# Performance work log

Hardware: AMD Instinct MI355X
Metric: run time of the kernel (lower is better)

The kernel has to match this reference:

```python
import jax, jax.numpy as jnp
import numpy as np

B, T, D = 16, 4096, 768          # batch, tokens, hidden
N_BOX = 1024                      # total boxes across batch
MAX_BBOX = 128                    # cfg.MODEL.MAX_BBOX_NUM
DIM_DETR = 256                    # DETR feature dim (features[:,1:])


def _lin(k, din, dout):
    kw, kb = jax.random.split(k)
    s = 1.0 / np.sqrt(din)
    W = jax.random.uniform(kw, (dout, din), minval=-s, maxval=s, dtype=jnp.float32)
    b = jax.random.uniform(kb, (dout,), minval=-s, maxval=s, dtype=jnp.float32)
    return W, b


def setup_inputs() -> dict:
    key = jax.random.key(0)
    ks = jax.random.split(key, 10)
    inputs = jax.random.normal(ks[0], (B, T, D), dtype=jnp.float32)
    img = jnp.sort(jax.random.randint(ks[1], (N_BOX,), 0, B))
    rest = jax.random.randint(ks[2], (N_BOX, 4), 0, 224)
    bboxes = jnp.concatenate([img[:, None], rest], axis=1).astype(jnp.int32)
    features = jax.random.normal(ks[3], (N_BOX, 1 + DIM_DETR), dtype=jnp.float32)
    t1w, t1b = _lin(ks[4], D, D)      # transform layer 1
    t2w, t2b = _lin(ks[5], D, D)      # transform layer 2
    d1w, d1b = _lin(ks[6], D, D)      # deep_trans layer 1
    d2w, d2b = _lin(ks[7], D, D)      # deep_trans layer 2
    k8a, k8b = jax.random.split(ks[8])
    m1w, m1b = _lin(k8a, DIM_DETR, D) # mlp layer 1 (256->768)
    m2w, m2b = _lin(k8b, D, D)        # mlp layer 2
    pw, pb = _lin(ks[9], 2 * D, D)    # projection (1536->768)
    return dict(inputs=inputs, bboxes=bboxes, features=features,
                t1w=t1w, t1b=t1b, t2w=t2w, t2b=t2b,
                d1w=d1w, d1b=d1b, d2w=d2w, d2b=d2b,
                m1w=m1w, m1b=m1b, m2w=m2w, m2b=m2b,
                pw=pw, pb=pb)


def reference(inputs, bboxes, features, t1w, t1b, t2w, t2b,
              d1w, d1b, d2w, d2b, m1w, m1b, m2w, m2b, pw, pb):
    x = inputs.mean(axis=1)                                    # [B, D]
    ret_x = jax.nn.relu(x @ d1w.T + d1b) @ d2w.T + d2b         # deep_trans
    xt = jax.nn.relu(x @ t1w.T + t1b) @ t2w.T + t2b            # transform
    img = bboxes[:, 0]                                          # [N] image idx per box
    x_boxes = xt[img]                                           # broadcast image feat to its boxes
    fm = jax.nn.relu(features[:, 1:] @ m1w.T + m1b) @ m2w.T + m2b  # DETR mlp
    h = jnp.concatenate([x_boxes, fm], axis=1) @ pw.T + pb      # [N, D]
    # ragged pad: scatter each box into slot (img, rank-within-image)
    counts = jax.ops.segment_sum(jnp.ones((N_BOX,), jnp.int32), img, num_segments=B)
    offsets = jnp.cumsum(counts) - counts                       # exclusive cumsum (boxes sorted by img)
    pos = jnp.arange(N_BOX) - offsets[img]
    vis_output = jnp.zeros((B, MAX_BBOX, D), h.dtype).at[img, pos].set(h)
    att_mask = (jnp.arange(MAX_BBOX)[None, :] < counts[:, None]).astype(jnp.float32)
    return vis_output, att_mask, ret_x
```

## Files before the change

kernel.cpp:

```cpp
#include <hip/hip_runtime.h>

#define B_ 16
#define T_ 4096
#define D_ 768
#define NBOX 1024
#define MAXBB 128
#define DDETR 256

typedef unsigned short u16;
typedef short bf16x8 __attribute__((ext_vector_type(8)));
typedef float f32x4 __attribute__((ext_vector_type(4)));

__device__ __forceinline__ void split_bf(float f, u16& h, u16& l) {
    unsigned u = __builtin_bit_cast(unsigned, f);
    unsigned r = u + 0x7fffu + ((u >> 16) & 1u);
    u16 hb = (u16)(r >> 16);
    float hf = __builtin_bit_cast(float, (unsigned)hb << 16);
    float lf = f - hf;
    unsigned ul = __builtin_bit_cast(unsigned, lf);
    unsigned rl = ul + 0x7fffu + ((ul >> 16) & 1u);
    h = hb; l = (u16)(rl >> 16);
}

__global__ __launch_bounds__(192) void k_mean_partial(const float4* __restrict__ in4,
                                                      float4* __restrict__ part4) {
    int blk = blockIdx.x;
    int b = blk >> 6, c = blk & 63;
    int t = threadIdx.x;
    const float4* base = in4 + (size_t)b * (T_ * D_ / 4) + (size_t)c * (64 * D_ / 4);
    float4 s = {0.f, 0.f, 0.f, 0.f};
    #pragma unroll 4
    for (int r = 0; r < 64; ++r) {
        float4 v = base[(size_t)r * 192 + t];
        s.x += v.x; s.y += v.y; s.z += v.z; s.w += v.w;
    }
    part4[(size_t)blk * 192 + t] = s;
}

__global__ __launch_bounds__(96) void k_mean_final_pack(const float* __restrict__ part,
                                                        u16* __restrict__ xph, u16* __restrict__ xpl) {
    int b = blockIdx.x;
    int kc = threadIdx.x;
    f32x4 s0 = {0,0,0,0}, s1 = {0,0,0,0};
    for (int c = 0; c < 64; ++c) {
        const float* p = part + ((size_t)(b * 64 + c)) * D_ + kc * 8;
        s0 += *(const f32x4*)p;
        s1 += *(const f32x4*)(p + 4);
    }
    const float inv = 1.0f / T_;
    bf16x8 hv, lv;
    #pragma unroll
    for (int j = 0; j < 4; ++j) {
        u16 h, l;
        split_bf(s0[j] * inv, h, l); hv[j] = (short)h; lv[j] = (short)l;
        split_bf(s1[j] * inv, h, l); hv[4 + j] = (short)h; lv[4 + j] = (short)l;
    }
    size_t off = ((size_t)kc * 16 + b) * 8;
    *(bf16x8*)(xph + off) = hv;
    *(bf16x8*)(xpl + off) = lv;
}

struct WDesc { const float* src; u16* hi; u16* lo; int N; int K; };
struct WPack7 { WDesc d[7]; };

__global__ __launch_bounds__(256) void k_pack_w(WPack7 ws) {
    WDesc d = ws.d[blockIdx.y];
    int idx = blockIdx.x * 256 + threadIdx.x;
    int Kc = d.K >> 3;
    int total = d.N * Kc;
    if (idx >= total) return;
    int n = idx / Kc, kc = idx - n * Kc;
    const float* s = d.src + (size_t)n * d.K + kc * 8;
    f32x4 v0 = *(const f32x4*)s, v1 = *(const f32x4*)(s + 4);
    bf16x8 hv, lv;
    #pragma unroll
    for (int j = 0; j < 4; ++j) {
        u16 h, l;
        split_bf(v0[j], h, l); hv[j] = (short)h; lv[j] = (short)l;
        split_bf(v1[j], h, l); hv[4 + j] = (short)h; lv[4 + j] = (short)l;
    }
    size_t off = ((size_t)(n >> 4) * Kc + kc) * 128 + (n & 15) * 8;
    *(bf16x8*)(d.hi + off) = hv;
    *(bf16x8*)(d.lo + off) = lv;
}

__global__ __launch_bounds__(256) void k_pack_feat(const float* __restrict__ feat,
                                                   u16* __restrict__ fh, u16* __restrict__ fl) {
    int idx = blockIdx.x * 256 + threadIdx.x;
    if (idx >= NBOX * 32) return;
    int i = idx >> 5, kc = idx & 31;
    const float* s = feat + (size_t)i * 257 + 1 + kc * 8;
    bf16x8 hv, lv;
    #pragma unroll
    for (int j = 0; j < 8; ++j) {
        u16 h, l;
        split_bf(s[j], h, l); hv[j] = (short)h; lv[j] = (short)l;
    }
    size_t off = ((size_t)(i >> 4) * 32 + kc) * 128 + (i & 15) * 8;
    *(bf16x8*)(fh + off) = hv;
    *(bf16x8*)(fl + off) = lv;
}

__global__ __launch_bounds__(256) void k_mfma(const u16* __restrict__ Ahi, const u16* __restrict__ Alo,
                                              const u16* __restrict__ Whi, const u16* __restrict__ Wlo,
                                              float* __restrict__ P, int Kc, int kcLen, int nks) {
    int z = blockIdx.z;
    int term = z / nks, ks = z - term * nks;
    const u16* A = (term == 2) ? Alo : Ahi;
    const u16* W = (term == 1) ? Wlo : Whi;
    int lane = threadIdx.x & 63, w = threadIdx.x >> 6;
    int wm = w >> 1, wn = w & 1;
    int mt0 = blockIdx.y * 8 + wm * 4;
    int nt0 = blockIdx.x * 8 + wn * 4;
    int kc0 = ks * kcLen;
    int nk = kcLen >> 2;

    const u16* Ap = A + ((size_t)mt0 * Kc + kc0) * 128 + lane * 8;
    const u16* Wp = W + ((size_t)nt0 * Kc + kc0) * 128 + lane * 8;
    size_t astr = (size_t)Kc * 128;

    bf16x8 a[4], b[4];
    #pragma unroll
    for (int i = 0; i < 4; ++i) {
        a[i] = *(const bf16x8*)(Ap + i * astr);
        b[i] = *(const bf16x8*)(Wp + i * astr);
    }
    f32x4 acc[16];
    #pragma unroll
    for (int i = 0; i < 16; ++i) acc[i] = (f32x4){0.f, 0.f, 0.f, 0.f};

    for (int k = 0; k < nk; ++k) {
        bf16x8 an[4], bn[4];
        if (k + 1 < nk) {
            #pragma unroll
            for (int i = 0; i < 4; ++i) {
                an[i] = *(const bf16x8*)(Ap + i * astr + (size_t)(k + 1) * 512);
                bn[i] = *(const bf16x8*)(Wp + i * astr + (size_t)(k + 1) * 512);
            }
        }
        #pragma unroll
        for (int i = 0; i < 4; ++i)
            #pragma unroll
            for (int j = 0; j < 4; ++j)
                acc[i * 4 + j] = __builtin_amdgcn_mfma_f32_16x16x32_bf16(a[i], b[j], acc[i * 4 + j], 0, 0, 0);
        #pragma unroll
        for (int i = 0; i < 4; ++i) { a[i] = an[i]; b[i] = bn[i]; }
    }

    float* Pz = P + (size_t)z * (1024 * 768);
    int rb = (lane >> 4) * 4, cb = lane & 15;
    #pragma unroll
    for (int i = 0; i < 4; ++i)
        #pragma unroll
        for (int j = 0; j < 4; ++j) {
            int row = (mt0 + i) * 16 + rb;
            int col = (nt0 + j) * 16 + cb;
            float* p = Pz + (size_t)row * 768 + col;
            f32x4 v = acc[i * 4 + j];
            #pragma unroll
            for (int r = 0; r < 4; ++r) p[(size_t)r * 768] = v[r];
        }
}

template<int RELU>
__global__ __launch_bounds__(256) void k_epi_pack(const float* __restrict__ P, int NS,
                                                  const float* __restrict__ bias,
                                                  u16* __restrict__ dhi, u16* __restrict__ dlo,
                                                  int KcDst, int kcOff) {
    int idx = blockIdx.x * 256 + threadIdx.x;
    int m = idx / 96, kc = idx - m * 96;
    const float* p0 = P + (size_t)m * 768 + kc * 8;
    f32x4 s0 = *(const f32x4*)p0, s1 = *(const f32x4*)(p0 + 4);
    for (int z = 1; z < NS; ++z) {
        const float* p = p0 + (size_t)z * (1024 * 768);
        s0 += *(const f32x4*)p; s1 += *(const f32x4*)(p + 4);
    }
    s0 += *(const f32x4*)(bias + kc * 8);
    s1 += *(const f32x4*)(bias + kc * 8 + 4);
    bf16x8 hv, lv;
    #pragma unroll
    for (int j = 0; j < 4; ++j) {
        float v0 = RELU ? fmaxf(s0[j], 0.f) : s0[j];
        float v1 = RELU ? fmaxf(s1[j], 0.f) : s1[j];
        u16 h, l;
        split_bf(v0, h, l); hv[j] = (short)h; lv[j] = (short)l;
        split_bf(v1, h, l); hv[4 + j] = (short)h; lv[4 + j] = (short)l;
    }
    size_t off = ((size_t)(m >> 4) * KcDst + kcOff + kc) * 128 + (m & 15) * 8;
    *(bf16x8*)(dhi + off) = hv;
    *(bf16x8*)(dlo + off) = lv;
}

__global__ __launch_bounds__(256) void k_epi_f32(const float* __restrict__ P, int NS,
                                                 const float* __restrict__ bias,
                                                 float* __restrict__ C) {
    int idx = blockIdx.x * 256 + threadIdx.x;
    int m = idx / 192, c4 = idx - m * 192;
    size_t off = (size_t)m * 768 + c4 * 4;
    f32x4 s = *(const f32x4*)(P + off);
    for (int z = 1; z < NS; ++z) s += *(const f32x4*)(P + (size_t)z * (1024 * 768) + off);
    s += *(const f32x4*)(bias + c4 * 4);
    *(f32x4*)(C + off) = s;
}

__global__ __launch_bounds__(256) void k_small(const u16* __restrict__ A0h, const u16* __restrict__ A0l,
                                               const u16* __restrict__ A1h, const u16* __restrict__ A1l,
                                               const u16* __restrict__ W0h, const u16* __restrict__ W0l,
                                               const u16* __restrict__ W1h, const u16* __restrict__ W1l,
                                               float* __restrict__ Ps) {
    int z = blockIdx.y;
    int term = z >> 2, ks = z & 3;
    int lane = threadIdx.x & 63, w = threadIdx.x >> 6;
    int nt0 = blockIdx.x * 16 + w * 4;
    int path = nt0 >= 48;
    int ntp = nt0 - path * 48;
    const u16* Ah = path ? A1h : A0h;
    const u16* Al = path ? A1l : A0l;
    const u16* Wh = path ? W1h : W0h;
    const u16* Wl = path ? W1l : W0l;
    const u16* A = (term == 2) ? Al : Ah;
    const u16* W = (term == 1) ? Wl : Wh;
    int kc0 = ks * 24;

    const u16* Ap = A + (size_t)kc0 * 128 + lane * 8;
    const u16* Wp = W + ((size_t)ntp * 96 + kc0) * 128 + lane * 8;

    f32x4 acc[4];
    #pragma unroll
    for (int i = 0; i < 4; ++i) acc[i] = (f32x4){0.f, 0.f, 0.f, 0.f};

    #pragma unroll
    for (int k = 0; k < 6; ++k) {
        bf16x8 a = *(const bf16x8*)(Ap + (size_t)k * 512);
        bf16x8 b[4];
        #pragma unroll
        for (int j = 0; j < 4; ++j)
            b[j] = *(const bf16x8*)(Wp + (size_t)j * 96 * 128 + (size_t)k * 512);
        #pragma unroll
        for (int j = 0; j < 4; ++j)
            acc[j] = __builtin_amdgcn_mfma_f32_16x16x32_bf16(a, b[j], acc[j], 0, 0, 0);
    }

    float* Pz = Ps + (size_t)z * (16 * 1536);
    int rb = (lane >> 4) * 4, cb = lane & 15;
    #pragma unroll
    for (int j = 0; j < 4; ++j) {
        int col = (nt0 + j) * 16 + cb;
        float* p = Pz + (size_t)rb * 1536 + col;
        f32x4 v = acc[j];
        #pragma unroll
        for (int r = 0; r < 4; ++r) p[(size_t)r * 1536] = v[r];
    }
}

__global__ __launch_bounds__(256) void k_sepi1(const float* __restrict__ Ps,
                                               const float* __restrict__ d1b, const float* __restrict__ t1b,
                                               u16* __restrict__ xh, u16* __restrict__ xl) {
    int idx = blockIdx.x * 256 + threadIdx.x;
    int r = idx / 192, cc = idx - r * 192;
    size_t base = (size_t)r * 1536 + cc * 8;
    f32x4 s0 = {0,0,0,0}, s1 = {0,0,0,0};
    for (int z = 0; z < 12; ++z) {
        const float* p = Ps + (size_t)z * (16 * 1536) + base;
        s0 += *(const f32x4*)p; s1 += *(const f32x4*)(p + 4);
    }
    int path = cc >= 96;
    int ccp = cc - path * 96;
    const float* bias = (path ? t1b : d1b) + ccp * 8;
    s0 += *(const f32x4*)bias;
    s1 += *(const f32x4*)(bias + 4);
    bf16x8 hv, lv;
    #pragma unroll
    for (int j = 0; j < 4; ++j) {
        u16 h, l;
        split_bf(fmaxf(s0[j], 0.f), h, l); hv[j] = (short)h; lv[j] = (short)l;
        split_bf(fmaxf(s1[j], 0.f), h, l); hv[4 + j] = (short)h; lv[4 + j] = (short)l;
    }
    size_t off = (size_t)path * 12288 + (size_t)ccp * 128 + r * 8;
    *(bf16x8*)(xh + off) = hv;
    *(bf16x8*)(xl + off) = lv;
}

__global__ __launch_bounds__(256) void k_sepi2(const float* __restrict__ Ps,
                                               const float* __restrict__ d2b, const float* __restrict__ t2b,
                                               float* __restrict__ retx,
                                               u16* __restrict__ xth, u16* __restrict__ xtl) {
    int idx = blockIdx.x * 256 + threadIdx.x;
    int r = idx / 192, cc = idx - r * 192;
    size_t base = (size_t)r * 1536 + cc * 8;
    f32x4 s0 = {0,0,0,0}, s1 = {0,0,0,0};
    for (int z = 0; z < 12; ++z) {
        const float* p = Ps + (size_t)z * (16 * 1536) + base;
        s0 += *(const f32x4*)p; s1 += *(const f32x4*)(p + 4);
    }
    int path = cc >= 96;
    int ccp = cc - path * 96;
    const float* bias = (path ? t2b : d2b) + ccp * 8;
    s0 += *(const f32x4*)bias;
    s1 += *(const f32x4*)(bias + 4);
    if (!path) {
        float* o = retx + (size_t)r * 768 + ccp * 8;
        *(f32x4*)o = s0;
        *(f32x4*)(o + 4) = s1;
    } else {
        bf16x8 hv, lv;
        #pragma unroll
        for (int j = 0; j < 4; ++j) {
            u16 h, l;
            split_bf(s0[j], h, l); hv[j] = (short)h; lv[j] = (short)l;
            split_bf(s1[j], h, l); hv[4 + j] = (short)h; lv[4 + j] = (short)l;
        }
        size_t off = (size_t)ccp * 128 + r * 8;
        *(bf16x8*)(xth + off) = hv;
        *(bf16x8*)(xtl + off) = lv;
    }
}

__global__ __launch_bounds__(256) void k_gather_pack(const u16* __restrict__ xth, const u16* __restrict__ xtl,
                                                     const int* __restrict__ bboxes,
                                                     u16* __restrict__ hxh, u16* __restrict__ hxl) {
    int idx = blockIdx.x * 256 + threadIdx.x;
    int i = idx / 96, kc = idx - i * 96;
    int img = bboxes[i * 5];
    size_t soff = ((size_t)kc * 16 + img) * 8;
    size_t doff = ((size_t)(i >> 4) * 192 + kc) * 128 + (i & 15) * 8;
    *(bf16x8*)(hxh + doff) = *(const bf16x8*)(xth + soff);
    *(bf16x8*)(hxl + doff) = *(const bf16x8*)(xtl + soff);
}

__global__ __launch_bounds__(256) void k_meta(const int* __restrict__ bboxes,
                                              int* __restrict__ cnt_g, int* __restrict__ off_g,
                                              float* __restrict__ att) {
    __shared__ int cnt[B_];
    __shared__ int off[B_];
    int tid = threadIdx.x;
    if (tid < B_) cnt[tid] = 0;
    __syncthreads();
    for (int i = tid; i < NBOX; i += 256) atomicAdd(&cnt[bboxes[i * 5]], 1);
    __syncthreads();
    if (tid == 0) {
        int acc = 0;
        for (int b = 0; b < B_; ++b) { off[b] = acc; acc += cnt[b]; }
    }
    __syncthreads();
    if (tid < B_) { cnt_g[tid] = cnt[tid]; off_g[tid] = off[tid]; }
    for (int j = tid; j < B_ * MAXBB; j += 256) {
        int b = j >> 7, p = j & 127;
        att[j] = (p < cnt[b]) ? 1.0f : 0.0f;
    }
}

__global__ __launch_bounds__(256) void k_vis(const float* __restrict__ h,
                                             const int* __restrict__ cnt,
                                             const int* __restrict__ off,
                                             float* __restrict__ vis) {
    int idx = blockIdx.x * 256 + threadIdx.x;
    int slot = idx / 192, d = idx - slot * 192;
    int b = slot >> 7, p = slot & 127;
    float4 v = {0.f, 0.f, 0.f, 0.f};
    if (p < cnt[b]) v = *(const float4*)&h[(size_t)(off[b] + p) * D_ + d * 4];
    *(float4*)&vis[(size_t)slot * D_ + d * 4] = v;
}

extern "C" void kernel_launch(void* const* d_in, const int* in_sizes, int n_in,
                              void* d_out, int out_size, void* d_ws, size_t ws_size,
                              hipStream_t stream) {
    const float* inputs   = (const float*)d_in[0];
    const int*   bboxes   = (const int*)d_in[1];
    const float* features = (const float*)d_in[2];
    const float* t1w = (const float*)d_in[3];
    const float* t1b = (const float*)d_in[4];
    const float* t2w = (const float*)d_in[5];
    const float* t2b = (const float*)d_in[6];
    const float* d1w = (const float*)d_in[7];
    const float* d1b = (const float*)d_in[8];
    const float* d2w = (const float*)d_in[9];
    const float* d2b = (const float*)d_in[10];
    const float* m1w = (const float*)d_in[11];
    const float* m1b = (const float*)d_in[12];
    const float* m2w = (const float*)d_in[13];
    const float* m2b = (const float*)d_in[14];
    const float* pw  = (const float*)d_in[15];
    const float* pb  = (const float*)d_in[16];

    float* out  = (float*)d_out;
    float* vis  = out;
    float* att  = out + 1572864;
    float* retx = out + 1574912;

    float* wsf  = (float*)d_ws;
    float* part = wsf;
    float* P    = wsf + 786432;
    float* Ps   = P + 12 * 786432;
    float* h    = Ps + 294912;
    int*   cnt  = (int*)(h + 786432);
    int*   off  = cnt + 16;
    u16*   sb   = (u16*)(off + 48);

    u16* t1wh = sb;              u16* t1wl = t1wh + 589824;
    u16* t2wh = t1wl + 589824;   u16* t2wl = t2wh + 589824;
    u16* d1wh = t2wl + 589824;   u16* d1wl = d1wh + 589824;
    u16* d2wh = d1wl + 589824;   u16* d2wl = d2wh + 589824;
    u16* m1wh = d2wl + 589824;   u16* m1wl = m1wh + 196608;
    u16* m2wh = m1wl + 196608;   u16* m2wl = m2wh + 589824;
    u16* pwh  = m2wl + 589824;   u16* pwl  = pwh + 1179648;
    u16* feah = pwl + 1179648;   u16* feal = feah + 262144;
    u16* fm1h = feal + 262144;   u16* fm1l = fm1h + 786432;
    u16* hxh  = fm1l + 786432;   u16* hxl  = hxh + 1572864;
    u16* xph  = hxl + 1572864;   u16* xpl  = xph + 12288;
    u16* xch  = xpl + 12288;     u16* xcl  = xch + 24576;
    u16* xth  = xcl + 24576;     u16* xtl  = xth + 12288;

    k_meta<<<1, 256, 0, stream>>>(bboxes, cnt, off, att);

    k_mean_partial<<<B_ * 64, 192, 0, stream>>>((const float4*)inputs, (float4*)part);
    k_mean_final_pack<<<16, 96, 0, stream>>>(part, xph, xpl);

    WPack7 wp;
    wp.d[0] = {t1w, t1wh, t1wl, 768, 768};
    wp.d[1] = {t2w, t2wh, t2wl, 768, 768};
    wp.d[2] = {d1w, d1wh, d1wl, 768, 768};
    wp.d[3] = {d2w, d2wh, d2wl, 768, 768};
    wp.d[4] = {m1w, m1wh, m1wl, 768, 256};
    wp.d[5] = {m2w, m2wh, m2wl, 768, 768};
    wp.d[6] = {pw,  pwh,  pwl,  768, 1536};
    k_pack_w<<<dim3(576, 7), 256, 0, stream>>>(wp);
    k_pack_feat<<<128, 256, 0, stream>>>(features, feah, feal);

    k_small<<<dim3(6, 12), 256, 0, stream>>>(xph, xpl, xph, xpl,
                                             d1wh, d1wl, t1wh, t1wl, Ps);
    k_sepi1<<<12, 256, 0, stream>>>(Ps, d1b, t1b, xch, xcl);
    k_small<<<dim3(6, 12), 256, 0, stream>>>(xch, xcl, xch + 12288, xcl + 12288,
                                             d2wh, d2wl, t2wh, t2wl, Ps);
    k_sepi2<<<12, 256, 0, stream>>>(Ps, d2b, t2b, retx, xth, xtl);

    k_gather_pack<<<384, 256, 0, stream>>>(xth, xtl, bboxes, hxh, hxl);

    k_mfma<<<dim3(6, 8, 6), 256, 0, stream>>>(feah, feal, m1wh, m1wl, P, 32, 16, 2);
    k_epi_pack<1><<<384, 256, 0, stream>>>(P, 6, m1b, fm1h, fm1l, 96, 0);

    k_mfma<<<dim3(6, 8, 12), 256, 0, stream>>>(fm1h, fm1l, m2wh, m2wl, P, 96, 24, 4);
    k_epi_pack<0><<<384, 256, 0, stream>>>(P, 12, m2b, hxh, hxl, 192, 96);

    k_mfma<<<dim3(6, 8, 12), 256, 0, stream>>>(hxh, hxl, pwh, pwl, P, 192, 48, 4);
    k_epi_f32<<<768, 256, 0, stream>>>(P, 12, pb, h);

    k_vis<<<1536, 256, 0, stream>>>(h, cnt, off, vis);
}
```

Before: 426.1 us.

## Fuse split-K partials into GEMM epilogues and scatter directly into padded output

```diff
diff --git a/kernel.cpp b/kernel.cpp
--- a/kernel.cpp
+++ b/kernel.cpp
@@ -37,295 +37,283 @@
     part4[(size_t)blk * 192 + t] = s;
 }
 
-__global__ __launch_bounds__(96) void k_mean_final_pack(const float* __restrict__ part,
-                                                        u16* __restrict__ xph, u16* __restrict__ xpl) {
+__global__ __launch_bounds__(192) void k_mean_final(const float* __restrict__ part,
+                                                    u16* __restrict__ xph, u16* __restrict__ xpl) {
+    __shared__ float xm[768];
     int b = blockIdx.x;
-    int kc = threadIdx.x;
-    f32x4 s0 = {0,0,0,0}, s1 = {0,0,0,0};
-    for (int c = 0; c < 64; ++c) {
-        const float* p = part + ((size_t)(b * 64 + c)) * D_ + kc * 8;
-        s0 += *(const f32x4*)p;
-        s1 += *(const f32x4*)(p + 4);
-    }
+    int t = threadIdx.x;
+    f32x4 s = {0.f, 0.f, 0.f, 0.f};
+    #pragma unroll 4
+    for (int c = 0; c < 64; ++c)
+        s += *(const f32x4*)(part + ((size_t)(b * 64 + c)) * 768 + t * 4);
     const float inv = 1.0f / T_;
-    bf16x8 hv, lv;
-    #pragma unroll
-    for (int j = 0; j < 4; ++j) {
-        u16 h, l;
-        split_bf(s0[j] * inv, h, l); hv[j] = (short)h; lv[j] = (short)l;
-        split_bf(s1[j] * inv, h, l); hv[4 + j] = (short)h; lv[4 + j] = (short)l;
-    }
-    size_t off = ((size_t)kc * 16 + b) * 8;
-    *(bf16x8*)(xph + off) = hv;
-    *(bf16x8*)(xpl + off) = lv;
-}
-
-struct WDesc { const float* src; u16* hi; u16* lo; int N; int K; };
-struct WPack7 { WDesc d[7]; };
-
-__global__ __launch_bounds__(256) void k_pack_w(WPack7 ws) {
+    s *= inv;
+    *(f32x4*)(xm + t * 4) = s;
+    __syncthreads();
+    if (t < 96) {
+        const float* p = xm + t * 8;
+        bf16x8 hv, lv;
+        #pragma unroll
+        for (int j = 0; j < 8; ++j) {
+            u16 h, l;
+            split_bf(p[j], h, l); hv[j] = (short)h; lv[j] = (short)l;
+        }
+        size_t off = ((size_t)t * 16 + b) * 8;
+        *(bf16x8*)(xph + off) = hv;
+        *(bf16x8*)(xpl + off) = lv;
+    }
+}
+
+struct WDesc { const float* src; u16* hi; u16* lo; int N; int K; int stride; int vec; };
+struct WPack8 { WDesc d[8]; };
+
+__global__ __launch_bounds__(256) void k_pack_w(WPack8 ws) {
     WDesc d = ws.d[blockIdx.y];
     int idx = blockIdx.x * 256 + threadIdx.x;
     int Kc = d.K >> 3;
     int total = d.N * Kc;
     if (idx >= total) return;
     int n = idx / Kc, kc = idx - n * Kc;
-    const float* s = d.src + (size_t)n * d.K + kc * 8;
-    f32x4 v0 = *(const f32x4*)s, v1 = *(const f32x4*)(s + 4);
+    const float* s = d.src + (size_t)n * d.stride + kc * 8;
+    float v[8];
+    if (d.vec) {
+        f32x4 v0 = *(const f32x4*)s, v1 = *(const f32x4*)(s + 4);
+        #pragma unroll
+        for (int j = 0; j < 4; ++j) { v[j] = v0[j]; v[4 + j] = v1[j]; }
+    } else {
+        #pragma unroll
+        for (int j = 0; j < 8; ++j) v[j] = s[j];
+    }
     bf16x8 hv, lv;
     #pragma unroll
-    for (int j = 0; j < 4; ++j) {
+    for (int j = 0; j < 8; ++j) {
         u16 h, l;
-        split_bf(v0[j], h, l); hv[j] = (short)h; lv[j] = (short)l;
-        split_bf(v1[j], h, l); hv[4 + j] = (short)h; lv[4 + j] = (short)l;
+        split_bf(v[j], h, l); hv[j] = (short)h; lv[j] = (short)l;
     }
     size_t off = ((size_t)(n >> 4) * Kc + kc) * 128 + (n & 15) * 8;
     *(bf16x8*)(d.hi + off) = hv;
     *(bf16x8*)(d.lo + off) = lv;
 }
 
-__global__ __launch_bounds__(256) void k_pack_feat(const float* __restrict__ feat,
-                                                   u16* __restrict__ fh, u16* __restrict__ fl) {
-    int idx = blockIdx.x * 256 + threadIdx.x;
-    if (idx >= NBOX * 32) return;
-    int i = idx >> 5, kc = idx & 31;
-    const float* s = feat + (size_t)i * 257 + 1 + kc * 8;
-    bf16x8 hv, lv;
-    #pragma unroll
-    for (int j = 0; j < 8; ++j) {
-        u16 h, l;
-        split_bf(s[j], h, l); hv[j] = (short)h; lv[j] = (short)l;
-    }
-    size_t off = ((size_t)(i >> 4) * 32 + kc) * 128 + (i & 15) * 8;
-    *(bf16x8*)(fh + off) = hv;
-    *(bf16x8*)(fl + off) = lv;
-}
-
-__global__ __launch_bounds__(256) void k_mfma(const u16* __restrict__ Ahi, const u16* __restrict__ Alo,
+template<int LAYER>
+__global__ __launch_bounds__(256) void k_small(const u16* __restrict__ Ah, const u16* __restrict__ Al,
+                                               const u16* __restrict__ W0h, const u16* __restrict__ W0l,
+                                               const u16* __restrict__ W1h, const u16* __restrict__ W1l,
+                                               const float* __restrict__ b0, const float* __restrict__ b1,
+                                               u16* __restrict__ dsth, u16* __restrict__ dstl,
+                                               float* __restrict__ retx) {
+    int lane = threadIdx.x & 63, w = threadIdx.x >> 6;
+    int lrow = lane & 15, lch = lane >> 4;
+    int c0 = blockIdx.x * 256 + w * 64;
+    int path = c0 >= 768;
+    int c0p = c0 - path * 768;
+    const u16* Wh = path ? W1h : W0h;
+    const u16* Wl = path ? W1l : W0l;
+    const u16* Axh = Ah + (LAYER == 2 ? (size_t)path * 12288 : 0);
+    const u16* Axl = Al + (LAYER == 2 ? (size_t)path * 12288 : 0);
+    size_t aoff = (size_t)lane * 8;
+    int nt0 = c0p >> 4;
+    size_t woff[4];
+    #pragma unroll
+    for (int j = 0; j < 4; ++j) woff[j] = ((size_t)(nt0 + j) * 96) * 128 + lane * 8;
+
+    f32x4 acc[4];
+    #pragma unroll
+    for (int j = 0; j < 4; ++j) acc[j] = (f32x4){0.f, 0.f, 0.f, 0.f};
+
+    bf16x8 ca[2], cb[2][4], na[2], nb[2][4];
+    auto LB = [&](int tb, bf16x8 (&a)[2], bf16x8 (&bb)[2][4]) {
+        int term = tb / 12, kb = tb - term * 12;
+        const u16* A = (term == 2) ? Axl : Axh;
+        const u16* Wt = (term == 1) ? Wl : Wh;
+        #pragma unroll
+        for (int s = 0; s < 2; ++s) {
+            int k = kb * 2 + s;
+            a[s] = *(const bf16x8*)(A + (size_t)k * 512 + aoff);
+            #pragma unroll
+            for (int j = 0; j < 4; ++j)
+                bb[s][j] = *(const bf16x8*)(Wt + woff[j] + (size_t)k * 512);
+        }
+    };
+
+    LB(0, ca, cb);
+    for (int tb = 0; tb < 36; ++tb) {
+        if (tb + 1 < 36) LB(tb + 1, na, nb);
+        #pragma unroll
+        for (int s = 0; s < 2; ++s)
+            #pragma unroll
+            for (int j = 0; j < 4; ++j)
+                acc[j] = __builtin_amdgcn_mfma_f32_16x16x32_bf16(ca[s], cb[s][j], acc[j], 0, 0, 0);
+        #pragma unroll
+        for (int s = 0; s < 2; ++s) {
+            ca[s] = na[s];
+            #pragma unroll
+            for (int j = 0; j < 4; ++j) cb[s][j] = nb[s][j];
+        }
+    }
+
+    __shared__ float lds[4][16][72];
+    const float* bias = path ? b1 : b0;
+    #pragma unroll
+    for (int j = 0; j < 4; ++j) {
+        float bv = bias[c0p + j * 16 + lrow];
+        #pragma unroll
+        for (int r = 0; r < 4; ++r) {
+            float x = acc[j][r] + bv;
+            if (LAYER == 1) x = fmaxf(x, 0.f);
+            lds[w][lch * 4 + r][j * 16 + lrow] = x;
+        }
+    }
+    __syncthreads();
+    #pragma unroll
+    for (int it = 0; it < 2; ++it) {
+        int task = it * 64 + lane;
+        int row = task >> 3, kcl = task & 7;
+        const float* p = &lds[w][row][kcl * 8];
+        if (LAYER == 2 && !path) {
+            float* o = retx + (size_t)row * 768 + c0 + kcl * 8;
+            *(f32x4*)o = *(const f32x4*)p;
+            *(f32x4*)(o + 4) = *(const f32x4*)(p + 4);
+        } else {
+            bf16x8 hv, lv;
+            #pragma unroll
+            for (int jj = 0; jj < 8; ++jj) {
+                u16 h, l;
+                split_bf(p[jj], h, l); hv[jj] = (short)h; lv[jj] = (short)l;
+            }
+            int kcg = (c0p >> 3) + kcl;
+            size_t off = (LAYER == 1 ? (size_t)path * 12288 : 0) + ((size_t)kcg * 16 + row) * 8;
+            *(bf16x8*)(dsth + off) = hv;
+            *(bf16x8*)(dstl + off) = lv;
+        }
+    }
+}
+
+template<int MODE>
+__global__ __launch_bounds__(256) void k_gemm(const u16* __restrict__ Ahi, const u16* __restrict__ Alo,
+                                              const u16* __restrict__ Xth, const u16* __restrict__ Xtl,
                                               const u16* __restrict__ Whi, const u16* __restrict__ Wlo,
-                                              float* __restrict__ P, int Kc, int kcLen, int nks) {
-    int z = blockIdx.z;
-    int term = z / nks, ks = z - term * nks;
-    const u16* A = (term == 2) ? Alo : Ahi;
-    const u16* W = (term == 1) ? Wlo : Whi;
+                                              const float* __restrict__ bias,
+                                              u16* __restrict__ Dhi, u16* __restrict__ Dlo,
+                                              int KcD, int kcOff,
+                                              float* __restrict__ vis, const int* __restrict__ bbx,
+                                              const int* __restrict__ offs, int Kc) {
     int lane = threadIdx.x & 63, w = threadIdx.x >> 6;
     int wm = w >> 1, wn = w & 1;
-    int mt0 = blockIdx.y * 8 + wm * 4;
-    int nt0 = blockIdx.x * 8 + wn * 4;
-    int kc0 = ks * kcLen;
-    int nk = kcLen >> 2;
-
-    const u16* Ap = A + ((size_t)mt0 * Kc + kc0) * 128 + lane * 8;
-    const u16* Wp = W + ((size_t)nt0 * Kc + kc0) * 128 + lane * 8;
-    size_t astr = (size_t)Kc * 128;
-
-    bf16x8 a[4], b[4];
-    #pragma unroll
-    for (int i = 0; i < 4; ++i) {
-        a[i] = *(const bf16x8*)(Ap + i * astr);
-        b[i] = *(const bf16x8*)(Wp + i * astr);
-    }
-    f32x4 acc[16];
-    #pragma unroll
-    for (int i = 0; i < 16; ++i) acc[i] = (f32x4){0.f, 0.f, 0.f, 0.f};
-
-    for (int k = 0; k < nk; ++k) {
-        bf16x8 an[4], bn[4];
-        if (k + 1 < nk) {
-            #pragma unroll
-            for (int i = 0; i < 4; ++i) {
-                an[i] = *(const bf16x8*)(Ap + i * astr + (size_t)(k + 1) * 512);
-                bn[i] = *(const bf16x8*)(Wp + i * astr + (size_t)(k + 1) * 512);
+    int m0 = blockIdx.y * 128 + wm * 64;
+    int n0 = blockIdx.x * 64 + wn * 32;
+    int mt0 = m0 >> 4, nt0 = n0 >> 4;
+    int lrow = lane & 15, lch = lane >> 4;
+
+    int AKc = (MODE == 2) ? 96 : Kc;
+    size_t aoff[4], boff[2], xoff[4];
+    #pragma unroll
+    for (int i = 0; i < 4; ++i) aoff[i] = ((size_t)(mt0 + i) * AKc) * 128 + lane * 8;
+    #pragma unroll
+    for (int j = 0; j < 2; ++j) boff[j] = ((size_t)(nt0 + j) * Kc) * 128 + lane * 8;
+    if (MODE == 2) {
+        #pragma unroll
+        for (int i = 0; i < 4; ++i)
+            xoff[i] = (size_t)lch * 128 + (size_t)bbx[(m0 + i * 16 + lrow) * 5] * 8;
+    }
+
+    int nk = Kc >> 2;
+    int NB = nk >> 1;
+    int TB = 3 * NB;
+
+    f32x4 acc[4][2];
+    #pragma unroll
+    for (int i = 0; i < 4; ++i)
+        #pragma unroll
+        for (int j = 0; j < 2; ++j) acc[i][j] = (f32x4){0.f, 0.f, 0.f, 0.f};
+
+    bf16x8 ca[2][4], cb[2][2], na[2][4], nb[2][2];
+    auto LB = [&](int tb, bf16x8 (&a)[2][4], bf16x8 (&b)[2][2]) {
+        int term = tb / NB, kb = tb - term * NB;
+        const u16* Wt = (term == 1) ? Wlo : Whi;
+        #pragma unroll
+        for (int s = 0; s < 2; ++s) {
+            int k = kb * 2 + s;
+            if (MODE == 2 && k < 24) {
+                const u16* Xs = (term == 2) ? Xtl : Xth;
+                #pragma unroll
+                for (int i = 0; i < 4; ++i)
+                    a[s][i] = *(const bf16x8*)(Xs + (size_t)k * 512 + xoff[i]);
+            } else {
+                const u16* As = (term == 2) ? Alo : Ahi;
+                int kk = (MODE == 2) ? k - 24 : k;
+                #pragma unroll
+                for (int i = 0; i < 4; ++i)
+                    a[s][i] = *(const bf16x8*)(As + aoff[i] + (size_t)kk * 512);
             }
-        }
-        #pragma unroll
-        for (int i = 0; i < 4; ++i)
-            #pragma unroll
-            for (int j = 0; j < 4; ++j)
-                acc[i * 4 + j] = __builtin_amdgcn_mfma_f32_16x16x32_bf16(a[i], b[j], acc[i * 4 + j], 0, 0, 0);
-        #pragma unroll
-        for (int i = 0; i < 4; ++i) { a[i] = an[i]; b[i] = bn[i]; }
-    }
-
-    float* Pz = P + (size_t)z * (1024 * 768);
-    int rb = (lane >> 4) * 4, cb = lane & 15;
-    #pragma unroll
-    for (int i = 0; i < 4; ++i)
-        #pragma unroll
-        for (int j = 0; j < 4; ++j) {
-            int row = (mt0 + i) * 16 + rb;
-            int col = (nt0 + j) * 16 + cb;
-            float* p = Pz + (size_t)row * 768 + col;
-            f32x4 v = acc[i * 4 + j];
-            #pragma unroll
-            for (int r = 0; r < 4; ++r) p[(size_t)r * 768] = v[r];
-        }
-}
-
-template<int RELU>
-__global__ __launch_bounds__(256) void k_epi_pack(const float* __restrict__ P, int NS,
-                                                  const float* __restrict__ bias,
-                                                  u16* __restrict__ dhi, u16* __restrict__ dlo,
-                                                  int KcDst, int kcOff) {
-    int idx = blockIdx.x * 256 + threadIdx.x;
-    int m = idx / 96, kc = idx - m * 96;
-    const float* p0 = P + (size_t)m * 768 + kc * 8;
-    f32x4 s0 = *(const f32x4*)p0, s1 = *(const f32x4*)(p0 + 4);
-    for (int z = 1; z < NS; ++z) {
-        const float* p = p0 + (size_t)z * (1024 * 768);
-        s0 += *(const f32x4*)p; s1 += *(const f32x4*)(p + 4);
-    }
-    s0 += *(const f32x4*)(bias + kc * 8);
-    s1 += *(const f32x4*)(bias + kc * 8 + 4);
-    bf16x8 hv, lv;
-    #pragma unroll
-    for (int j = 0; j < 4; ++j) {
-        float v0 = RELU ? fmaxf(s0[j], 0.f) : s0[j];
-        float v1 = RELU ? fmaxf(s1[j], 0.f) : s1[j];
-        u16 h, l;
-        split_bf(v0, h, l); hv[j] = (short)h; lv[j] = (short)l;
-        split_bf(v1, h, l); hv[4 + j] = (short)h; lv[4 + j] = (short)l;
-    }
-    size_t off = ((size_t)(m >> 4) * KcDst + kcOff + kc) * 128 + (m & 15) * 8;
-    *(bf16x8*)(dhi + off) = hv;
-    *(bf16x8*)(dlo + off) = lv;
-}
-
-__global__ __launch_bounds__(256) void k_epi_f32(const float* __restrict__ P, int NS,
-                                                 const float* __restrict__ bias,
-                                                 float* __restrict__ C) {
-    int idx = blockIdx.x * 256 + threadIdx.x;
-    int m = idx / 192, c4 = idx - m * 192;
-    size_t off = (size_t)m * 768 + c4 * 4;
-    f32x4 s = *(const f32x4*)(P + off);
-    for (int z = 1; z < NS; ++z) s += *(const f32x4*)(P + (size_t)z * (1024 * 768) + off);
-    s += *(const f32x4*)(bias + c4 * 4);
-    *(f32x4*)(C + off) = s;
-}
-
-__global__ __launch_bounds__(256) void k_small(const u16* __restrict__ A0h, const u16* __restrict__ A0l,
-                                               const u16* __restrict__ A1h, const u16* __restrict__ A1l,
-                                               const u16* __restrict__ W0h, const u16* __restrict__ W0l,
-                                               const u16* __restrict__ W1h, const u16* __restrict__ W1l,
-                                               float* __restrict__ Ps) {
-    int z = blockIdx.y;
-    int term = z >> 2, ks = z & 3;
-    int lane = threadIdx.x & 63, w = threadIdx.x >> 6;
-    int nt0 = blockIdx.x * 16 + w * 4;
-    int path = nt0 >= 48;
-    int ntp = nt0 - path * 48;
-    const u16* Ah = path ? A1h : A0h;
-    const u16* Al = path ? A1l : A0l;
-    const u16* Wh = path ? W1h : W0h;
-    const u16* Wl = path ? W1l : W0l;
-    const u16* A = (term == 2) ? Al : Ah;
-    const u16* W = (term == 1) ? Wl : Wh;
-    int kc0 = ks * 24;
-
-    const u16* Ap = A + (size_t)kc0 * 128 + lane * 8;
-    const u16* Wp = W + ((size_t)ntp * 96 + kc0) * 128 + lane * 8;
-
-    f32x4 acc[4];
-    #pragma unroll
-    for (int i = 0; i < 4; ++i) acc[i] = (f32x4){0.f, 0.f, 0.f, 0.f};
-
-    #pragma unroll
-    for (int k = 0; k < 6; ++k) {
-        bf16x8 a = *(const bf16x8*)(Ap + (size_t)k * 512);
-        bf16x8 b[4];
-        #pragma unroll
-        for (int j = 0; j < 4; ++j)
-            b[j] = *(const bf16x8*)(Wp + (size_t)j * 96 * 128 + (size_t)k * 512);
-        #pragma unroll
-        for (int j = 0; j < 4; ++j)
-            acc[j] = __builtin_amdgcn_mfma_f32_16x16x32_bf16(a, b[j], acc[j], 0, 0, 0);
-    }
-
-    float* Pz = Ps + (size_t)z * (16 * 1536);
-    int rb = (lane >> 4) * 4, cb = lane & 15;
-    #pragma unroll
-    for (int j = 0; j < 4; ++j) {
-        int col = (nt0 + j) * 16 + cb;
-        float* p = Pz + (size_t)rb * 1536 + col;
-        f32x4 v = acc[j];
-        #pragma unroll
-        for (int r = 0; r < 4; ++r) p[(size_t)r * 1536] = v[r];
-    }
-}
-
-__global__ __launch_bounds__(256) void k_sepi1(const float* __restrict__ Ps,
-                                               const float* __restrict__ d1b, const float* __restrict__ t1b,
-                                               u16* __restrict__ xh, u16* __restrict__ xl) {
-    int idx = blockIdx.x * 256 + threadIdx.x;
-    int r = idx / 192, cc = idx - r * 192;
-    size_t base = (size_t)r * 1536 + cc * 8;
-    f32x4 s0 = {0,0,0,0}, s1 = {0,0,0,0};
-    for (int z = 0; z < 12; ++z) {
-        const float* p = Ps + (size_t)z * (16 * 1536) + base;
-        s0 += *(const f32x4*)p; s1 += *(const f32x4*)(p + 4);
-    }
-    int path = cc >= 96;
-    int ccp = cc - path * 96;
-    const float* bias = (path ? t1b : d1b) + ccp * 8;
-    s0 += *(const f32x4*)bias;
-    s1 += *(const f32x4*)(bias + 4);
-    bf16x8 hv, lv;
-    #pragma unroll
-    for (int j = 0; j < 4; ++j) {
-        u16 h, l;
-        split_bf(fmaxf(s0[j], 0.f), h, l); hv[j] = (short)h; lv[j] = (short)l;
-        split_bf(fmaxf(s1[j], 0.f), h, l); hv[4 + j] = (short)h; lv[4 + j] = (short)l;
-    }
-    size_t off = (size_t)path * 12288 + (size_t)ccp * 128 + r * 8;
-    *(bf16x8*)(xh + off) = hv;
-    *(bf16x8*)(xl + off) = lv;
-}
-
-__global__ __launch_bounds__(256) void k_sepi2(const float* __restrict__ Ps,
-                                               const float* __restrict__ d2b, const float* __restrict__ t2b,
-                                               float* __restrict__ retx,
-                                               u16* __restrict__ xth, u16* __restrict__ xtl) {
-    int idx = blockIdx.x * 256 + threadIdx.x;
-    int r = idx / 192, cc = idx - r * 192;
-    size_t base = (size_t)r * 1536 + cc * 8;
-    f32x4 s0 = {0,0,0,0}, s1 = {0,0,0,0};
-    for (int z = 0; z < 12; ++z) {
-        const float* p = Ps + (size_t)z * (16 * 1536) + base;
-        s0 += *(const f32x4*)p; s1 += *(const f32x4*)(p + 4);
-    }
-    int path = cc >= 96;
-    int ccp = cc - path * 96;
-    const float* bias = (path ? t2b : d2b) + ccp * 8;
-    s0 += *(const f32x4*)bias;
-    s1 += *(const f32x4*)(bias + 4);
-    if (!path) {
-        float* o = retx + (size_t)r * 768 + ccp * 8;
-        *(f32x4*)o = s0;
-        *(f32x4*)(o + 4) = s1;
-    } else {
-        bf16x8 hv, lv;
-        #pragma unroll
-        for (int j = 0; j < 4; ++j) {
-            u16 h, l;
-            split_bf(s0[j], h, l); hv[j] = (short)h; lv[j] = (short)l;
-            split_bf(s1[j], h, l); hv[4 + j] = (short)h; lv[4 + j] = (short)l;
-        }
-        size_t off = (size_t)ccp * 128 + r * 8;
-        *(bf16x8*)(xth + off) = hv;
-        *(bf16x8*)(xtl + off) = lv;
-    }
-}
-
-__global__ __launch_bounds__(256) void k_gather_pack(const u16* __restrict__ xth, const u16* __restrict__ xtl,
-                                                     const int* __restrict__ bboxes,
-                                                     u16* __restrict__ hxh, u16* __restrict__ hxl) {
-    int idx = blockIdx.x * 256 + threadIdx.x;
-    int i = idx / 96, kc = idx - i * 96;
-    int img = bboxes[i * 5];
-    size_t soff = ((size_t)kc * 16 + img) * 8;
-    size_t doff = ((size_t)(i >> 4) * 192 + kc) * 128 + (i & 15) * 8;
-    *(bf16x8*)(hxh + doff) = *(const bf16x8*)(xth + soff);
-    *(bf16x8*)(hxl + doff) = *(const bf16x8*)(xtl + soff);
+            #pragma unroll
+            for (int j = 0; j < 2; ++j)
+                b[s][j] = *(const bf16x8*)(Wt + boff[j] + (size_t)k * 512);
+        }
+    };
+
+    LB(0, ca, cb);
+    for (int tb = 0; tb < TB; ++tb) {
+        if (tb + 1 < TB) LB(tb + 1, na, nb);
+        #pragma unroll
+        for (int s = 0; s < 2; ++s)
+            #pragma unroll
+            for (int i = 0; i < 4; ++i)
+                #pragma unroll
+                for (int j = 0; j < 2; ++j)
+                    acc[i][j] = __builtin_amdgcn_mfma_f32_16x16x32_bf16(ca[s][i], cb[s][j], acc[i][j], 0, 0, 0);
+        #pragma unroll
+        for (int s = 0; s < 2; ++s) {
+            #pragma unroll
+            for (int i = 0; i < 4; ++i) ca[s][i] = na[s][i];
+            #pragma unroll
+            for (int j = 0; j < 2; ++j) cb[s][j] = nb[s][j];
+        }
+    }
+
+    __shared__ float lds[4][64][40];
+    #pragma unroll
+    for (int j = 0; j < 2; ++j) {
+        float bv = bias[n0 + j * 16 + lrow];
+        #pragma unroll
+        for (int i = 0; i < 4; ++i) {
+            #pragma unroll
+            for (int r = 0; r < 4; ++r) {
+                float x = acc[i][j][r] + bv;
+                if (MODE == 0) x = fmaxf(x, 0.f);
+                lds[w][i * 16 + lch * 4 + r][j * 16 + lrow] = x;
+            }
+        }
+    }
+    __syncthreads();
+    #pragma unroll
+    for (int it = 0; it < 4; ++it) {
+        int task = it * 64 + lane;
+        int row = task >> 2, kcl = task & 3;
+        const float* p = &lds[w][row][kcl * 8];
+        if (MODE == 2) {
+            int box = m0 + row;
+            int b = bbx[box * 5];
+            int pp = box - offs[b];
+            if (pp < MAXBB) {
+                float* o = vis + ((size_t)(b * MAXBB + pp)) * 768 + n0 + kcl * 8;
+                *(f32x4*)o = *(const f32x4*)p;
+                *(f32x4*)(o + 4) = *(const f32x4*)(p + 4);
+            }
+        } else {
+            bf16x8 hv, lv;
+            #pragma unroll
+            for (int jj = 0; jj < 8; ++jj) {
+                u16 h, l;
+                split_bf(p[jj], h, l); hv[jj] = (short)h; lv[jj] = (short)l;
+            }
+            int m = m0 + row;
+            int kcg = (n0 >> 3) + kcl;
+            size_t off = ((size_t)(m >> 4) * KcD + kcOff + kcg) * 128 + (m & 15) * 8;
+            *(bf16x8*)(Dhi + off) = hv;
+            *(bf16x8*)(Dlo + off) = lv;
+        }
+    }
 }
 
 __global__ __launch_bounds__(256) void k_meta(const int* __restrict__ bboxes,
@@ -350,16 +338,9 @@
     }
 }
 
-__global__ __launch_bounds__(256) void k_vis(const float* __restrict__ h,
-                                             const int* __restrict__ cnt,
-                                             const int* __restrict__ off,
-                                             float* __restrict__ vis) {
+__global__ __launch_bounds__(256) void k_viszero(f32x4* __restrict__ vis4) {
     int idx = blockIdx.x * 256 + threadIdx.x;
-    int slot = idx / 192, d = idx - slot * 192;
-    int b = slot >> 7, p = slot & 127;
-    float4 v = {0.f, 0.f, 0.f, 0.f};
-    if (p < cnt[b]) v = *(const float4*)&h[(size_t)(off[b] + p) * D_ + d * 4];
-    *(float4*)&vis[(size_t)slot * D_ + d * 4] = v;
+    vis4[idx] = (f32x4){0.f, 0.f, 0.f, 0.f};
 }
 
 extern "C" void kernel_launch(void* const* d_in, const int* in_sizes, int n_in,
@@ -390,10 +371,7 @@
 
     float* wsf  = (float*)d_ws;
     float* part = wsf;
-    float* P    = wsf + 786432;
-    float* Ps   = P + 12 * 786432;
-    float* h    = Ps + 294912;
-    int*   cnt  = (int*)(h + 786432);
+    int*   cnt  = (int*)(wsf + 786432);
     int*   off  = cnt + 16;
     u16*   sb   = (u16*)(off + 48);
 
@@ -406,44 +384,40 @@
     u16* pwh  = m2wl + 589824;   u16* pwl  = pwh + 1179648;
     u16* feah = pwl + 1179648;   u16* feal = feah + 262144;
     u16* fm1h = feal + 262144;   u16* fm1l = fm1h + 786432;
-    u16* hxh  = fm1l + 786432;   u16* hxl  = hxh + 1572864;
-    u16* xph  = hxl + 1572864;   u16* xpl  = xph + 12288;
+    u16* fmh  = fm1l + 786432;   u16* fml  = fmh + 786432;
+    u16* xph  = fml + 786432;    u16* xpl  = xph + 12288;
     u16* xch  = xpl + 12288;     u16* xcl  = xch + 24576;
     u16* xth  = xcl + 24576;     u16* xtl  = xth + 12288;
 
     k_meta<<<1, 256, 0, stream>>>(bboxes, cnt, off, att);
+    k_viszero<<<1536, 256, 0, stream>>>((f32x4*)vis);
 
     k_mean_partial<<<B_ * 64, 192, 0, stream>>>((const float4*)inputs, (float4*)part);
-    k_mean_final_pack<<<16, 96, 0, stream>>>(part, xph, xpl);
-
-    WPack7 wp;
-    wp.d[0] = {t1w, t1wh, t1wl, 768, 768};
-    wp.d[1] = {t2w, t2wh, t2wl, 768, 768};
-    wp.d[2] = {d1w, d1wh, d1wl, 768, 768};
-    wp.d[3] = {d2w, d2wh, d2wl, 768, 768};
-    wp.d[4] = {m1w, m1wh, m1wl, 768, 256};
-    wp.d[5] = {m2w, m2wh, m2wl, 768, 768};
-    wp.d[6] = {pw,  pwh,  pwl,  768, 1536};
-    k_pack_w<<<dim3(576, 7), 256, 0, stream>>>(wp);
-    k_pack_feat<<<128, 256, 0, stream>>>(features, feah, feal);
-
-    k_small<<<dim3(6, 12), 256, 0, stream>>>(xph, xpl, xph, xpl,
-                                             d1wh, d1wl, t1wh, t1wl, Ps);
-    k_sepi1<<<12, 256, 0, stream>>>(Ps, d1b, t1b, xch, xcl);
-    k_small<<<dim3(6, 12), 256, 0, stream>>>(xch, xcl, xch + 12288, xcl + 12288,
-                                             d2wh, d2wl, t2wh, t2wl, Ps);
-    k_sepi2<<<12, 256, 0, stream>>>(Ps, d2b, t2b, retx, xth, xtl);
-
-    k_gather_pack<<<384, 256, 0, stream>>>(xth, xtl, bboxes, hxh, hxl);
-
-    k_mfma<<<dim3(6, 8, 6), 256, 0, stream>>>(feah, feal, m1wh, m1wl, P, 32, 16, 2);
-    k_epi_pack<1><<<384, 256, 0, stream>>>(P, 6, m1b, fm1h, fm1l, 96, 0);
-
-    k_mfma<<<dim3(6, 8, 12), 256, 0, stream>>>(fm1h, fm1l, m2wh, m2wl, P, 96, 24, 4);
-    k_epi_pack<0><<<384, 256, 0, stream>>>(P, 12, m2b, hxh, hxl, 192, 96);
-
-    k_mfma<<<dim3(6, 8, 12), 256, 0, stream>>>(hxh, hxl, pwh, pwl, P, 192, 48, 4);
-    k_epi_f32<<<768, 256, 0, stream>>>(P, 12, pb, h);
-
-    k_vis<<<1536, 256, 0, stream>>>(h, cnt, off, vis);
-}
+    k_mean_final<<<16, 192, 0, stream>>>(part, xph, xpl);
+
+    WPack8 wp;
+    wp.d[0] = {t1w, t1wh, t1wl, 768, 768, 768, 1};
+    wp.d[1] = {t2w, t2wh, t2wl, 768, 768, 768, 1};
+    wp.d[2] = {d1w, d1wh, d1wl, 768, 768, 768, 1};
+    wp.d[3] = {d2w, d2wh, d2wl, 768, 768, 768, 1};
+    wp.d[4] = {m1w, m1wh, m1wl, 768, 256, 256, 1};
+    wp.d[5] = {m2w, m2wh, m2wl, 768, 768, 768, 1};
+    wp.d[6] = {pw,  pwh,  pwl,  768, 1536, 1536, 1};
+    wp.d[7] = {features + 1, feah, feal, 1024, 256, 257, 0};
+    k_pack_w<<<dim3(576, 8), 256, 0, stream>>>(wp);
+
+    k_small<1><<<6, 256, 0, stream>>>(xph, xpl, d1wh, d1wl, t1wh, t1wl,
+                                      d1b, t1b, xch, xcl, nullptr);
+    k_small<2><<<6, 256, 0, stream>>>(xch, xcl, d2wh, d2wl, t2wh, t2wl,
+                                      d2b, t2b, xth, xtl, retx);
+
+    k_gemm<0><<<dim3(12, 8), 256, 0, stream>>>(feah, feal, nullptr, nullptr,
+                                               m1wh, m1wl, m1b, fm1h, fm1l, 96, 0,
+                                               nullptr, nullptr, nullptr, 32);
+    k_gemm<1><<<dim3(12, 8), 256, 0, stream>>>(fm1h, fm1l, nullptr, nullptr,
+                                               m2wh, m2wl, m2b, fmh, fml, 96, 0,
+                                               nullptr, nullptr, nullptr, 96);
+    k_gemm<2><<<dim3(12, 8), 256, 0, stream>>>(fmh, fml, xth, xtl,
+                                               pwh, pwl, pb, nullptr, nullptr, 0, 0,
+                                               vis, bboxes, off, 192);
+}
```

After: 461.8 us. 8.4% more time.
